# Kernel tuning notes

Measured on AMD Instinct MI355X. Metric: run time of the kernel, lower is better.

The kernel has to match this reference:

```python
import jax, jax.numpy as jnp
import numpy as np

ATTN_SCALE = 0.12
HEAD_DIM = 128


def _rms_norm(x):
    # F.rms_norm with no weight; eps defaults to machine eps of dtype
    eps = jnp.asarray(jnp.finfo(x.dtype).eps, x.dtype)
    return x * jax.lax.rsqrt(jnp.mean(x * x, axis=-1, keepdims=True) + eps)


def _rope(x):
    # x: [B, T, H, D]; standard rotary over (first-half, second-half) pairs
    T, D = x.shape[1], x.shape[-1]
    half = D // 2
    inv_freq = 1.0 / (10000.0 ** (jnp.arange(half, dtype=jnp.float32) / half))
    ang = jnp.arange(T, dtype=jnp.float32)[:, None] * inv_freq[None, :]  # [T, half]
    cos = jnp.cos(ang)[None, :, None, :].astype(x.dtype)
    sin = jnp.sin(ang)[None, :, None, :].astype(x.dtype)
    x1, x2 = x[..., :half], x[..., half:]
    return jnp.concatenate([x1 * cos - x2 * sin, x1 * sin + x2 * cos], axis=-1)


def setup_inputs() -> dict:
    key = jax.random.key(0)
    ks = jax.random.split(key, 4)
    B, T, dim, H, hd = 4, 2048, 1024, 8, HEAD_DIM
    hdim = H * hd
    std = 0.5 * dim ** (-0.5)
    bound = (3.0 ** 0.5) * std
    return {
        "x": jax.random.normal(ks[0], (B, T, dim), jnp.float32),
        "ve": jax.random.normal(ks[1], (B, T, hdim), jnp.float32),
        "qkv_w": jax.random.uniform(ks[2], (3, hdim, dim), jnp.float32, -bound, bound),
        "lambdas": jnp.array([0.5, 0.5], jnp.float32),
        "c_proj_w": jax.random.normal(ks[3], (dim, hdim), jnp.float32) * (hdim ** -0.5),
        "c_proj_b": jnp.zeros((dim,), jnp.float32),
    }


def reference(x, ve, qkv_w, lambdas, c_proj_w, c_proj_b):
    B, T, dim = x.shape
    hdim = qkv_w.shape[1]
    hd = HEAD_DIM
    H = hdim // hd
    # fused QKV projection: [B,T,3,H,hd]
    qkv = jnp.einsum('btd,ehd->bteh', x, qkv_w.reshape(3 * hdim, dim).reshape(3 * H, hd, dim).reshape(3 * hdim // hd, hd, dim))
    qkv = jnp.einsum('btd,fd->btf', x, qkv_w.reshape(3 * hdim, dim)).reshape(B, T, 3, H, hd)
    q, k, v = qkv[:, :, 0], qkv[:, :, 1], qkv[:, :, 2]  # each [B,T,H,hd]
    q, k = _rms_norm(q), _rms_norm(k)
    q, k = _rope(q), _rope(k)
    v = lambdas[0] * v + lambdas[1] * ve.reshape(B, T, H, hd)
    # causal SDPA with custom scale
    scores = jnp.einsum('bthd,bshd->bhts', q, k) * ATTN_SCALE  # [B,H,T,T]
    causal = jnp.tril(jnp.ones((T, T), dtype=bool))
    scores = jnp.where(causal[None, None], scores, jnp.finfo(scores.dtype).min)
    p = jax.nn.softmax(scores, axis=-1)
    y = jnp.einsum('bhts,bshd->bthd', p, v).reshape(B, T, hdim)
    return y @ c_proj_w.T + c_proj_b
```

## Files before the change

### kernel.cpp

```cpp
#include <hip/hip_runtime.h>
#include <math.h>

typedef unsigned short u16;
typedef short bf16x8 __attribute__((ext_vector_type(8)));
typedef u16 u16x2 __attribute__((ext_vector_type(2)));
typedef u16 u16x4 __attribute__((ext_vector_type(4)));
typedef u16 u16x8 __attribute__((ext_vector_type(8)));
typedef float f32x2 __attribute__((ext_vector_type(2)));
typedef float f32x4 __attribute__((ext_vector_type(4)));
typedef float f32x16 __attribute__((ext_vector_type(16)));

typedef __attribute__((address_space(1))) const void gvoid_t;
typedef __attribute__((address_space(3))) void lvoid_t;

__device__ __forceinline__ u16 f2bf(float f) {
  union { float f; unsigned u; } v; v.f = f;
  unsigned r = v.u + 0x7fffu + ((v.u >> 16) & 1u);
  return (u16)(r >> 16);
}
__device__ __forceinline__ float bf2f(u16 h) {
  union { unsigned u; float f; } v; v.u = ((unsigned)h) << 16;
  return v.f;
}
__device__ __forceinline__ f32x4 mfma16(bf16x8 a, bf16x8 b, f32x4 c) {
  return __builtin_amdgcn_mfma_f32_16x16x32_bf16(a, b, c, 0, 0, 0);
}
__device__ __forceinline__ f32x16 mfma32(bf16x8 a, bf16x8 b, f32x16 c) {
  return __builtin_amdgcn_mfma_f32_32x32x16_bf16(a, b, c, 0, 0, 0);
}
__device__ __forceinline__ void gload_lds16(const void* g, void* l) {
  __builtin_amdgcn_global_load_lds((gvoid_t*)g, (lvoid_t*)l, 16, 0, 0);
}
__device__ __forceinline__ unsigned cvtpk_bf16(float lo, float hi) {
  unsigned r;
  asm("v_cvt_pk_bf16_f32 %0, %1, %2" : "=v"(r) : "v"(lo), "v"(hi));
  return r;
}
__device__ __forceinline__ void pswap32(unsigned& a, unsigned& b) {
  asm("v_permlane32_swap_b32 %0, %1" : "+v"(a), "+v"(b));
}

#if __has_builtin(__builtin_amdgcn_exp2f)
#define EXPW(x) __builtin_amdgcn_exp2f(x)
#define SCALE_W 0.17312354f
#define DEFER_THR 11.5415603f
#else
#define EXPW(x) __expf(x)
#define SCALE_W 0.12f
#define DEFER_THR 8.0f
#endif

#define BAR() __builtin_amdgcn_s_barrier()
#define WAITLGKM()                          \
  asm volatile("s_waitcnt lgkmcnt(0)");     \
  __builtin_amdgcn_sched_barrier(0)
#define WAITVMC(N)                                    \
  do {                                                \
    __builtin_amdgcn_s_waitcnt(0x0F70 | (N));         \
    __builtin_amdgcn_sched_barrier(0);                \
  } while (0)

__constant__ int C_ST[24] = {15,15,7,14,14,13,13,6,12,12,11,11,5,10,10,4,9,9,8,8,3,2,1,0};
__constant__ int C_HF[24] = {0,1,-1,0,1,0,1,-1,0,1,0,1,-1,0,1,-1,0,1,0,1,-1,-1,-1,-1};

__global__ __launch_bounds__(256) void cvt_bf16_kernel(const float* __restrict__ in,
                                                       u16* __restrict__ out, int n4) {
  int i = blockIdx.x * 256 + threadIdx.x;
  if (i >= n4) return;
  f32x4 v = *(const f32x4*)(in + (size_t)i * 4);
  u16x4 o;
  o[0] = f2bf(v[0]); o[1] = f2bf(v[1]); o[2] = f2bf(v[2]); o[3] = f2bf(v[3]);
  *(u16x4*)(out + (size_t)i * 4) = o;
}

__global__ __launch_bounds__(256) void rope_tab_kernel(float* __restrict__ ct,
                                                       float* __restrict__ st) {
  int i = blockIdx.x * 256 + threadIdx.x;
  int t = i >> 6, j = i & 63;
  float inv = powf(10000.f, -(float)j * (1.0f / 64.0f));
  float ang = (float)t * inv;
  ct[i] = cosf(ang);
  st[i] = sinf(ang);
}

__global__ __launch_bounds__(512, 1) void gemm192_kernel(
    const u16* __restrict__ A, const u16* __restrict__ B, u16* __restrict__ C,
    int M, int N, int K, int nbn) {
  constexpr int WM = 128;
  constexpr int MI = 4;
  constexpr int NI = 3;
  constexpr int AR = 4;
  constexpr int NR = 7;
  __shared__ u16 Alds[2][256 * 64];
  __shared__ u16 Blds[2][192 * 64];
  int nwg = gridDim.x;
  int cpx = nwg >> 3;
  int bid = blockIdx.x;
  int swz = (bid & 7) * cpx + (bid >> 3);
  int bm = (swz & 3) + 4 * (swz / (4 * nbn));
  int bn = (swz >> 2) % nbn;
  size_t m0 = (size_t)bm * 256, n0 = (size_t)bn * 192;
  int tid = threadIdx.x, wid = tid >> 6, lane = tid & 63;
  int wr = wid >> 2, wc = wid & 3, l15 = lane & 15, l4 = lane >> 4;
  int srow = tid >> 3, sch = tid & 7;

  const u16* Abase = A + m0 * K;
  const u16* Bbase = B + n0 * K;

  f32x4 acc[8][NI];
#pragma unroll
  for (int m = 0; m < 8; m++)
#pragma unroll
    for (int n = 0; n < NI; n++) acc[m][n] = f32x4{0.f, 0.f, 0.f, 0.f};

  auto stageR = [&](int buf, int kt, int r) {
    if (r < AR) {
      int row = 64 * r + srow;
      gload_lds16(Abase + (size_t)row * K + kt * 64 + 8 * (sch ^ (row & 7)),
                  &Alds[buf][(64 * r + 8 * wid) * 64]);
    } else {
      int row = 64 * (r - AR) + srow;
      gload_lds16(Bbase + (size_t)row * K + kt * 64 + 8 * (sch ^ (row & 7)),
                  &Blds[buf][(64 * (r - AR) + 8 * wid) * 64]);
    }
  };
  auto rdA = [&](int buf, int half, bf16x8 (&a)[MI][2]) {
#pragma unroll
    for (int mi = 0; mi < MI; ++mi)
#pragma unroll
      for (int kk = 0; kk < 2; ++kk) {
        int row = WM * wr + 64 * half + 16 * mi + l15;
        a[mi][kk] = *(const bf16x8*)((const char*)(&Alds[buf][0]) + row * 128 +
                                     ((kk * 64 + 16 * l4) ^ ((row & 7) << 4)));
      }
  };
  auto rdB = [&](int buf, bf16x8 (&bb)[NI][2]) {
#pragma unroll
    for (int ni = 0; ni < NI; ++ni)
#pragma unroll
      for (int kk = 0; kk < 2; ++kk) {
        int row = 48 * wc + 16 * ni + l15;
        bb[ni][kk] = *(const bf16x8*)((const char*)(&Blds[buf][0]) + row * 128 +
                                      ((kk * 64 + 16 * l4) ^ ((row & 7) << 4)));
      }
  };

#define HALFM(AF, BF, QM)                                                 \
  do {                                                                    \
    __builtin_amdgcn_s_setprio(1);                                        \
    _Pragma("unroll") for (int mi = 0; mi < MI; ++mi)                     \
        _Pragma("unroll") for (int ni = 0; ni < NI; ++ni)                 \
            _Pragma("unroll") for (int kk = 0; kk < 2; ++kk)              \
                acc[4 * QM + mi][ni] =                                    \
        mfma16(AF[mi][kk], BF[ni][kk], acc[4 * QM + mi][ni]);             \
    __builtin_amdgcn_s_setprio(0);                                        \
  } while (0)

#pragma unroll
  for (int r = 0; r < NR; ++r) stageR(0, 0, r);
  WAITVMC(0);
  BAR();

  int nk = K >> 6;
  bf16x8 a[MI][2], b[NI][2];
  for (int t = 0; t < nk; ++t) {
    int buf = t & 1, nxt = buf ^ 1;
    bool pf = (t + 1 < nk);
    rdA(buf, 0, a);
    rdB(buf, b);
    if (pf) { stageR(nxt, t + 1, 0); stageR(nxt, t + 1, 1); stageR(nxt, t + 1, 2); stageR(nxt, t + 1, 3); }
    BAR();
    WAITLGKM();
    HALFM(a, b, 0);
    BAR();
    rdA(buf, 1, a);
    if (pf) { stageR(nxt, t + 1, 4); stageR(nxt, t + 1, 5); stageR(nxt, t + 1, 6); }
    BAR();
    WAITLGKM();
    HALFM(a, b, 1);
    WAITVMC(0);
    BAR();
  }

#pragma unroll
  for (int mi = 0; mi < 8; ++mi) {
#pragma unroll
    for (int ni = 0; ni < NI; ++ni) {
      size_t row = m0 + WM * wr + 16 * mi + 4 * l4;
      size_t col = n0 + 48 * wc + 16 * ni + l15;
#pragma unroll
      for (int i = 0; i < 4; ++i) {
        C[(row + i) * N + col] = f2bf(acc[mi][ni][i]);
      }
    }
  }
#undef HALFM
}

template <int BM, int OUTF32>
__global__ __launch_bounds__(512, 1) void gemm4p_kernel(
    const u16* __restrict__ A, const u16* __restrict__ B, void* __restrict__ C,
    const float* __restrict__ bias, int M, int N, int K, int nbn) {
  constexpr int WM = BM / 2;
  constexpr int MI = (WM / 32 > 0) ? WM / 32 : 1;
  constexpr int NACC = 2 * MI;
  constexpr int AR = BM / 64;
  constexpr int NR = AR + 4;
  constexpr int R0 = (NR + 2) / 3;
  constexpr int R1 = R0 + (NR - R0 + 1) / 2;
  __shared__ u16 Alds[2][BM * 64];
  __shared__ u16 Blds[2][256 * 64];
  int nwg = gridDim.x;
  int cpx = nwg >> 3;
  int bid = blockIdx.x;
  int swz = (bid & 7) * cpx + (bid >> 3);
  int bm = (swz & 3) + 4 * (swz / (4 * nbn));
  int bn = (swz >> 2) % nbn;
  size_t m0 = (size_t)bm * BM, n0 = (size_t)bn * 256;
  int tid = threadIdx.x, wid = tid >> 6, lane = tid & 63;
  int wr = wid >> 2, wc = wid & 3, l15 = lane & 15, l4 = lane >> 4;
  int srow = tid >> 3, sch = tid & 7;

  const u16* Abase = A + m0 * K;
  const u16* Bbase = B + n0 * K;

  f32x4 acc[NACC][4];
#pragma unroll
  for (int m = 0; m < NACC; m++)
#pragma unroll
    for (int n = 0; n < 4; n++) acc[m][n] = f32x4{0.f, 0.f, 0.f, 0.f};

  auto stageR = [&](int buf, int kt, int r) {
    if (r < AR) {
      int row = 64 * r + srow;
      gload_lds16(Abase + (size_t)row * K + kt * 64 + 8 * (sch ^ (row & 7)),
                  &Alds[buf][(64 * r + 8 * wid) * 64]);
    } else {
      int row = 64 * (r - AR) + srow;
      gload_lds16(Bbase + (size_t)row * K + kt * 64 + 8 * (sch ^ (row & 7)),
                  &Blds[buf][(64 * (r - AR) + 8 * wid) * 64]);
    }
  };
  auto rdA = [&](int buf, int qm, bf16x8 (&a)[MI][2]) {
#pragma unroll
    for (int mi = 0; mi < MI; ++mi)
#pragma unroll
      for (int kk = 0; kk < 2; ++kk) {
        int row = WM * wr + (WM / 2) * qm + 16 * mi + l15;
        a[mi][kk] = *(const bf16x8*)((const char*)(&Alds[buf][0]) + row * 128 +
                                     ((kk * 64 + 16 * l4) ^ ((row & 7) << 4)));
      }
  };
  auto rdB = [&](int buf, int qn, bf16x8 (&bb)[2][2]) {
#pragma unroll
    for (int ni = 0; ni < 2; ++ni)
#pragma unroll
      for (int kk = 0; kk < 2; ++kk) {
        int row = 64 * wc + 32 * qn + 16 * ni + l15;
        bb[ni][kk] = *(const bf16x8*)((const char*)(&Blds[buf][0]) + row * 128 +
                                      ((kk * 64 + 16 * l4) ^ ((row & 7) << 4)));
      }
  };

#define QUADX(AF, BF, QM, QN)                                             \
  do {                                                                    \
    __builtin_amdgcn_s_setprio(1);                                        \
    _Pragma("unroll") for (int mi = 0; mi < MI; ++mi)                     \
        _Pragma("unroll") for (int ni = 0; ni < 2; ++ni)                  \
            _Pragma("unroll") for (int kk = 0; kk < 2; ++kk)              \
                acc[MI * QM + mi][2 * QN + ni] =                          \
        mfma16(AF[mi][kk], BF[ni][kk], acc[MI * QM + mi][2 * QN + ni]);   \
    __builtin_amdgcn_s_setprio(0);                                        \
  } while (0)

#pragma unroll
  for (int r = 0; r < NR; ++r) stageR(0, 0, r);
  WAITVMC(0);
  BAR();

  int nk = K >> 6;
  bf16x8 a[MI][2], b0[2][2], b1[2][2];
  for (int t = 0; t < nk; ++t) {
    int buf = t & 1, nxt = buf ^ 1;
    bool pf = (t + 1 < nk);
    rdA(buf, 0, a);
    rdB(buf, 0, b0);
    if (pf) {
#pragma unroll
      for (int r = 0; r < R0; ++r) stageR(nxt, t + 1, r);
    }
    BAR();
    WAITLGKM();
    QUADX(a, b0, 0, 0);
    BAR();
    rdB(buf, 1, b1);
    if (pf) {
#pragma unroll
      for (int r = R0; r < R1; ++r) stageR(nxt, t + 1, r);
    }
    BAR();
    WAITLGKM();
    QUADX(a, b1, 0, 1);
    BAR();
    rdA(buf, 1, a);
    if (pf) {
#pragma unroll
      for (int r = R1; r < NR; ++r) stageR(nxt, t + 1, r);
    }
    BAR();
    WAITLGKM();
    QUADX(a, b0, 1, 0);
    BAR();
    QUADX(a, b1, 1, 1);
    WAITVMC(0);
    BAR();
  }

#pragma unroll
  for (int mi = 0; mi < NACC; ++mi) {
#pragma unroll
    for (int ni = 0; ni < 4; ++ni) {
      size_t row = m0 + WM * wr + 16 * mi + 4 * l4;
      size_t col = n0 + 64 * wc + 16 * ni + l15;
#pragma unroll
      for (int i = 0; i < 4; ++i) {
        float v = acc[mi][ni][i];
        if constexpr (OUTF32) {
          ((float*)C)[(row + i) * N + col] = v + bias[col];
        } else {
          ((u16*)C)[(row + i) * N + col] = f2bf(v);
        }
      }
    }
  }
#undef QUADX
}

__global__ __launch_bounds__(256) void transform_kernel(
    const u16* __restrict__ qkv, const float* __restrict__ ve,
    const float* __restrict__ lam, const float* __restrict__ ct,
    const float* __restrict__ st, u16* __restrict__ qn, u16* __restrict__ kn,
    u16* __restrict__ vt) {
  constexpr int T = 2048;
  __shared__ u16 vtile[64][136];
  int tt = blockIdx.x, bh = blockIdx.y;
  int b = bh >> 3, h = bh & 7;
  int tid = threadIdx.x, wid = tid >> 6, lane = tid & 63;
  int lsub = lane & 15, lrow = lane >> 4;
  float l0 = lam[0], l1 = lam[1];
  int d0 = 8 * lsub;
  float sgn = (lsub < 8) ? -1.f : 1.f;
  int jj = d0 & 63;
#pragma unroll
  for (int it = 0; it < 4; ++it) {
    int tl = wid * 16 + it * 4 + lrow;
    int t = tt * 64 + tl;
    size_t base = ((size_t)(b * T + t)) * 3072 + h * 128 + d0;
    u16x8 qraw = *(const u16x8*)(qkv + base);
    u16x8 kraw = *(const u16x8*)(qkv + base + 1024);
    u16x8 vraw = *(const u16x8*)(qkv + base + 2048);
    const float* vep = ve + ((size_t)(b * T + t)) * 1024 + h * 128 + d0;
    f32x4 ve0 = *(const f32x4*)(vep);
    f32x4 ve1 = *(const f32x4*)(vep + 4);
    float q[8], k[8];
    float sq = 0.f, sk = 0.f;
#pragma unroll
    for (int i = 0; i < 8; ++i) {
      q[i] = bf2f(qraw[i]); k[i] = bf2f(kraw[i]);
      sq += q[i] * q[i]; sk += k[i] * k[i];
    }
#pragma unroll
    for (int m = 1; m < 16; m <<= 1) {
      sq += __shfl_xor(sq, m);
      sk += __shfl_xor(sk, m);
    }
    float qs = rsqrtf(sq * (1.f / 128.f) + 1.1920929e-7f);
    float ks = rsqrtf(sk * (1.f / 128.f) + 1.1920929e-7f);
#pragma unroll
    for (int i = 0; i < 8; ++i) { q[i] *= qs; k[i] *= ks; }
    f32x4 c0 = *(const f32x4*)(ct + t * 64 + jj);
    f32x4 c1 = *(const f32x4*)(ct + t * 64 + jj + 4);
    f32x4 s0 = *(const f32x4*)(st + t * 64 + jj);
    f32x4 s1 = *(const f32x4*)(st + t * 64 + jj + 4);
    u16x8 oq, ok, ov;
#pragma unroll
    for (int i = 0; i < 8; ++i) {
      float qp = __shfl_xor(q[i], 8), kp = __shfl_xor(k[i], 8);
      float cc = (i < 4) ? c0[i & 3] : c1[i & 3];
      float ss = (i < 4) ? s0[i & 3] : s1[i & 3];
      oq[i] = f2bf(q[i] * cc + sgn * qp * ss);
      ok[i] = f2bf(k[i] * cc + sgn * kp * ss);
      float vv = (i < 4) ? ve0[i & 3] : ve1[i & 3];
      ov[i] = f2bf(l0 * bf2f(vraw[i]) + l1 * vv);
    }
    size_t orow = ((size_t)bh * T + t) * 128 + d0;
    *(u16x8*)(qn + orow) = oq;
    *(u16x8*)(kn + orow) = ok;
    *(u16x8*)&vtile[tl][d0] = ov;
  }
  __syncthreads();
#pragma unroll
  for (int it = 0; it < 4; ++it) {
    int ci = it * 256 + tid;
    int d = ci >> 3, c8 = ci & 7;
    u16x8 o;
#pragma unroll
    for (int u = 0; u < 8; u++) o[u] = vtile[c8 * 8 + u][d];
    *(u16x8*)(vt + ((size_t)bh * 128 + d) * T + tt * 64 + c8 * 8) = o;
  }
}

__global__ __launch_bounds__(256, 2) void attn_kernel(
    const u16* __restrict__ Qn, const u16* __restrict__ Kn,
    const u16* __restrict__ Vt, u16* __restrict__ Y,
    u16* __restrict__ pO, float* __restrict__ pml) {
  constexpr int T = 2048;
  __shared__ u16 Klds[2][64 * 128];
  __shared__ u16 Vlds[2][128 * 64];
  int bid = blockIdx.x;
  int c = bid >> 5;
  int bh = bid & 31;
  int st = C_ST[c];
  int half = C_HF[c];
  int kt0 = (half == 1) ? st + 1 : 0;
  int kt1 = (half == 0) ? st + 1 : 2 * st + 2;
  int b = bh >> 3, h = bh & 7;
  int tid = threadIdx.x, wid = tid >> 6, lane = tid & 63;
  int l31 = lane & 31, hh = lane >> 5;
  const u16* Qb = Qn + (size_t)bh * T * 128;
  const u16* Kb = Kn + (size_t)bh * T * 128;
  const u16* Vb = Vt + (size_t)bh * 128 * T;
  int q0w = st * 128 + wid * 32;
  int qmaxw = q0w + 31;
  int qg = q0w + l31;

  bf16x8 qf[8];
  {
    const u16* qr = Qb + (size_t)(q0w + l31) * 128 + 8 * hh;
#pragma unroll
    for (int ks = 0; ks < 8; ks++) qf[ks] = *(const bf16x8*)(qr + 16 * ks);
  }
  f32x16 acc[4];
#pragma unroll
  for (int mt = 0; mt < 4; mt++)
#pragma unroll
    for (int r = 0; r < 16; r++) acc[mt][r] = 0.f;
  float m_run = -1e30f, l_run = 0.f;

  auto stage = [&](int buf, int kt) {
#pragma unroll
    for (int it = 0; it < 4; ++it) {
      int id = wid * 256 + it * 64 + lane;
      int r = id >> 4, cc = id & 15;
      gload_lds16(Kb + (size_t)(kt * 64 + r) * 128 + 8 * (cc ^ (r & 7)),
                  &Klds[buf][(size_t)(wid * 256 + it * 64) * 8]);
      int rv = id >> 3, cv = id & 7;
      gload_lds16(Vb + (size_t)rv * T + kt * 64 + 8 * (cv ^ (rv & 7)),
                  &Vlds[buf][(size_t)(wid * 256 + it * 64) * 8]);
    }
  };

  int nsteps = kt1 - kt0;
  stage(0, kt0);

  for (int j = 0; j < nsteps; ++j) {
    int kt = kt0 + j;
    int cur = j & 1;
    if (j + 1 < nsteps) {
      stage(cur ^ 1, kt + 1);
      WAITVMC(8);
    } else {
      WAITVMC(0);
    }
    BAR();
    if (kt * 64 <= qmaxw) {
      const char* kb = (const char*)&Klds[cur][0];
      const char* vb = (const char*)&Vlds[cur][0];
      int rswz = (l31 & 7) << 4;
      f32x16 st0, st1;
#pragma unroll
      for (int r = 0; r < 16; r++) { st0[r] = 0.f; st1[r] = 0.f; }
      __builtin_amdgcn_s_setprio(1);
#pragma unroll
      for (int ks = 0; ks < 8; ks++) {
        bf16x8 kf0 = *(const bf16x8*)(kb + ((l31 * 256 + 32 * ks + 16 * hh) ^ rswz));
        bf16x8 kf1 = *(const bf16x8*)(kb + (((32 + l31) * 256 + 32 * ks + 16 * hh) ^ rswz));
        st0 = mfma32(kf0, qf[ks], st0);
        st1 = mfma32(kf1, qf[ks], st1);
      }
      __builtin_amdgcn_s_setprio(0);
      bool edge = (kt == (qmaxw >> 6));
      if (edge) {
#pragma unroll
        for (int r = 0; r < 16; r++) {
          int kvb = kt * 64 + (r & 3) + 8 * (r >> 2) + 4 * hh;
          if (kvb > qg) st0[r] = -1e30f;
          if (kvb + 32 > qg) st1[r] = -1e30f;
        }
      }
      float m8[8];
#pragma unroll
      for (int r = 0; r < 8; r++)
        m8[r] = fmaxf(fmaxf(st0[r], st0[r + 8]), fmaxf(st1[r], st1[r + 8]));
#pragma unroll
      for (int r = 0; r < 4; r++) m8[r] = fmaxf(m8[r], m8[r + 4]);
      float pm = fmaxf(fmaxf(m8[0], m8[1]), fmaxf(m8[2], m8[3]));
      pm = fmaxf(pm, __shfl_xor(pm, 32));
      float pmn = pm * SCALE_W;
      bool nos = __all(pmn <= m_run + DEFER_THR);
      float mnew = nos ? m_run : fmaxf(m_run, pmn);
      if (!nos) {
        float alpha = EXPW(m_run - mnew);
        l_run *= alpha;
#pragma unroll
        for (int mt = 0; mt < 4; mt++)
#pragma unroll
          for (int r = 0; r < 16; r++) acc[mt][r] *= alpha;
        m_run = mnew;
      }
      float sa = 0.f, sb = 0.f, sc = 0.f, sd = 0.f;
#pragma unroll
      for (int r = 0; r < 4; r++) {
        st0[r]      = EXPW(fmaf(st0[r],      SCALE_W, -mnew)); sa += st0[r];
        st0[r + 4]  = EXPW(fmaf(st0[r + 4],  SCALE_W, -mnew)); sb += st0[r + 4];
        st0[r + 8]  = EXPW(fmaf(st0[r + 8],  SCALE_W, -mnew)); sc += st0[r + 8];
        st0[r + 12] = EXPW(fmaf(st0[r + 12], SCALE_W, -mnew)); sd += st0[r + 12];
        st1[r]      = EXPW(fmaf(st1[r],      SCALE_W, -mnew)); sa += st1[r];
        st1[r + 4]  = EXPW(fmaf(st1[r + 4],  SCALE_W, -mnew)); sb += st1[r + 4];
        st1[r + 8]  = EXPW(fmaf(st1[r + 8],  SCALE_W, -mnew)); sc += st1[r + 8];
        st1[r + 12] = EXPW(fmaf(st1[r + 12], SCALE_W, -mnew)); sd += st1[r + 12];
      }
      float ps = (sa + sb) + (sc + sd);
      ps += __shfl_xor(ps, 32);
      l_run += ps;
      unsigned pA0[4], pB0[4], pA1[4], pB1[4];
#pragma unroll
      for (int rr = 0; rr < 4; rr++) {
        pA0[rr] = cvtpk_bf16(st0[4 * rr], st0[4 * rr + 1]);
        pB0[rr] = cvtpk_bf16(st0[4 * rr + 2], st0[4 * rr + 3]);
        pA1[rr] = cvtpk_bf16(st1[4 * rr], st1[4 * rr + 1]);
        pB1[rr] = cvtpk_bf16(st1[4 * rr + 2], st1[4 * rr + 3]);
      }
      bf16x8 pf[4];
#pragma unroll
      for (int ks2 = 0; ks2 < 4; ks2++) {
        int k1 = ks2 & 1;
        unsigned a0, b0, a1, b1;
        if (ks2 < 2) { a0 = pA0[2 * k1]; b0 = pA0[2 * k1 + 1]; a1 = pB0[2 * k1]; b1 = pB0[2 * k1 + 1]; }
        else         { a0 = pA1[2 * k1]; b0 = pA1[2 * k1 + 1]; a1 = pB1[2 * k1]; b1 = pB1[2 * k1 + 1]; }
        pswap32(a0, b0);
        pswap32(a1, b1);
        union { unsigned w[4]; bf16x8 v; } u;
        u.w[0] = a0; u.w[1] = a1; u.w[2] = b0; u.w[3] = b1;
        pf[ks2] = u.v;
      }
      __builtin_amdgcn_s_setprio(1);
#pragma unroll
      for (int mt = 0; mt < 4; mt++) {
        int row = 32 * mt + l31;
#pragma unroll
        for (int ks2 = 0; ks2 < 4; ks2++) {
          bf16x8 vf = *(const bf16x8*)(vb + ((row * 128 + 32 * ks2 + 16 * hh) ^ rswz));
          acc[mt] = mfma32(vf, pf[ks2], acc[mt]);
        }
      }
      __builtin_amdgcn_s_setprio(0);
    }
    BAR();
  }
  if (half < 0) {
    float linv = 1.f / l_run;
    size_t yrow = (size_t)b * T + q0w + l31;
    u16* yp = Y + yrow * 1024 + h * 128;
#pragma unroll
    for (int mt = 0; mt < 4; mt++) {
#pragma unroll
      for (int rr = 0; rr < 4; rr++) {
        u16x4 o;
#pragma unroll
        for (int i = 0; i < 4; i++) o[i] = f2bf(acc[mt][4 * rr + i] * linv);
        *(u16x4*)(yp + 32 * mt + 8 * rr + 4 * hh) = o;
      }
    }
  } else {
    int pidx = (((st - 8) << 5) + bh) * 2 + half;
    int qrow = wid * 32 + l31;
    u16* po = pO + (size_t)pidx * 16384 + (size_t)qrow * 128;
#pragma unroll
    for (int mt = 0; mt < 4; mt++) {
#pragma unroll
      for (int rr = 0; rr < 4; rr++) {
        u16x4 o;
#pragma unroll
        for (int i = 0; i < 4; i++) o[i] = f2bf(acc[mt][4 * rr + i]);
        *(u16x4*)(po + 32 * mt + 8 * rr + 4 * hh) = o;
      }
    }
    if (hh == 0) {
      pml[pidx * 256 + qrow] = m_run;
      pml[pidx * 256 + 128 + qrow] = l_run;
    }
  }
}

__global__ __launch_bounds__(256) void attn_merge_kernel(
    const u16* __restrict__ pO, const float* __restrict__ pml,
    u16* __restrict__ Y) {
  int blk = blockIdx.x;
  int st = 8 + (blk >> 5), bh = blk & 31;
  int b = bh >> 3, h = bh & 7;
  int tid = threadIdx.x;
  int row = tid >> 1, dh = tid & 1;
  int base = blk * 2;
  const u16* o1 = pO + (size_t)base * 16384 + (size_t)row * 128 + dh * 64;
  const u16* o2 = o1 + 16384;
  float m1 = pml[base * 256 + row], l1 = pml[base * 256 + 128 + row];
  float m2 = pml[(base + 1) * 256 + row], l2 = pml[(base + 1) * 256 + 128 + row];
  float m = fmaxf(m1, m2);
  float w1 = EXPW(m1 - m), w2 = EXPW(m2 - m);
  float inv = 1.f / (w1 * l1 + w2 * l2);
  w1 *= inv; w2 *= inv;
  u16* yp = Y + ((size_t)b * 2048 + 128 * st + row) * 1024 + h * 128 + dh * 64;
#pragma unroll
  for (int i = 0; i < 8; ++i) {
    u16x8 a = *(const u16x8*)(o1 + 8 * i);
    u16x8 cvec = *(const u16x8*)(o2 + 8 * i);
    u16x8 o;
#pragma unroll
    for (int j = 0; j < 8; ++j) o[j] = f2bf(w1 * bf2f(a[j]) + w2 * bf2f(cvec[j]));
    *(u16x8*)(yp + 8 * i) = o;
  }
}

extern "C" void kernel_launch(void* const* d_in, const int* in_sizes, int n_in,
                              void* d_out, int out_size, void* d_ws, size_t ws_size,
                              hipStream_t stream) {
  (void)in_sizes; (void)n_in; (void)out_size; (void)ws_size;
  const float* x = (const float*)d_in[0];
  const float* ve = (const float*)d_in[1];
  const float* qkvw = (const float*)d_in[2];
  const float* lam = (const float*)d_in[3];
  const float* cpw = (const float*)d_in[4];
  const float* cpb = (const float*)d_in[5];
  float* out = (float*)d_out;
  char* ws = (char*)d_ws;

  u16* xb   = (u16*)(ws + 0);
  u16* wqkv = (u16*)(ws + 16777216);
  u16* wp   = (u16*)(ws + 23068672);
  u16* qkv  = (u16*)(ws + 25165824);
  u16* qn   = (u16*)(ws + 75497472);
  u16* kn   = (u16*)(ws + 92274688);
  u16* vt   = (u16*)(ws + 109051904);
  float* ctab = (float*)(ws + 125829120);
  float* stab = (float*)(ws + 126353408);
  u16* y = xb;
  u16* pO = qkv;
  float* pml = (float*)(ws + 25165824 + 16777216);

  rope_tab_kernel<<<512, 256, 0, stream>>>(ctab, stab);
  cvt_bf16_kernel<<<8192, 256, 0, stream>>>(x, xb, 2097152);
  cvt_bf16_kernel<<<3072, 256, 0, stream>>>(qkvw, wqkv, 786432);
  cvt_bf16_kernel<<<1024, 256, 0, stream>>>(cpw, wp, 262144);
  gemm192_kernel<<<512, 512, 0, stream>>>(xb, wqkv, qkv, 8192, 3072, 1024, 16);
  transform_kernel<<<dim3(32, 32), 256, 0, stream>>>(qkv, ve, lam, ctab, stab, qn, kn, vt);
  attn_kernel<<<768, 256, 0, stream>>>(qn, kn, vt, y, pO, pml);
  attn_merge_kernel<<<256, 256, 0, stream>>>(pO, pml, y);
  gemm4p_kernel<64, 1><<<512, 512, 0, stream>>>(y, wp, out, cpb, 8192, 1024, 1024, 4);
}
```

Baseline: 203.7 us.

## Enlarge attention query tiles to 256 rows with 512-thread blocks and simplify GEMM prefetch

The attention kernel now processes 256 query rows per block with 8 waves, up from 128 rows with 4 waves. Each staged K/V tile is therefore reused by twice as many query rows, and the causal split/merge schedule, partial-output layout and merge kernel are rewritten to match. The output-projection GEMM also issues all next-tile prefetch loads at once instead of spreading them across three phases. The larger blocks halve the grid and may hurt load balance and occupancy, and issuing the whole prefetch up front can reduce overlap with compute.

```diff
diff --git a/kernel.cpp b/kernel.cpp
--- a/kernel.cpp
+++ b/kernel.cpp
@@ -60,8 +60,8 @@
     __builtin_amdgcn_sched_barrier(0);                \
   } while (0)
 
-__constant__ int C_ST[24] = {15,15,7,14,14,13,13,6,12,12,11,11,5,10,10,4,9,9,8,8,3,2,1,0};
-__constant__ int C_HF[24] = {0,1,-1,0,1,0,1,-1,0,1,0,1,-1,0,1,-1,0,1,0,1,-1,-1,-1,-1};
+__constant__ int C_ST2[12] = {7, 7, 3, 6, 6, 5, 5, 2, 4, 4, 1, 0};
+__constant__ int C_H2[12]  = {0, 1, -1, 0, 1, 0, 1, -1, 0, 1, -1, -1};
 
 __global__ __launch_bounds__(256) void cvt_bf16_kernel(const float* __restrict__ in,
                                                        u16* __restrict__ out, int n4) {
@@ -206,8 +206,6 @@
   constexpr int NACC = 2 * MI;
   constexpr int AR = BM / 64;
   constexpr int NR = AR + 4;
-  constexpr int R0 = (NR + 2) / 3;
-  constexpr int R1 = R0 + (NR - R0 + 1) / 2;
   __shared__ u16 Alds[2][BM * 64];
   __shared__ u16 Blds[2][256 * 64];
   int nwg = gridDim.x;
@@ -287,26 +285,18 @@
     rdB(buf, 0, b0);
     if (pf) {
 #pragma unroll
-      for (int r = 0; r < R0; ++r) stageR(nxt, t + 1, r);
+      for (int r = 0; r < NR; ++r) stageR(nxt, t + 1, r);
     }
     BAR();
     WAITLGKM();
     QUADX(a, b0, 0, 0);
     BAR();
     rdB(buf, 1, b1);
-    if (pf) {
-#pragma unroll
-      for (int r = R0; r < R1; ++r) stageR(nxt, t + 1, r);
-    }
     BAR();
     WAITLGKM();
     QUADX(a, b1, 0, 1);
     BAR();
     rdA(buf, 1, a);
-    if (pf) {
-#pragma unroll
-      for (int r = R1; r < NR; ++r) stageR(nxt, t + 1, r);
-    }
     BAR();
     WAITLGKM();
     QUADX(a, b0, 1, 0);
@@ -410,7 +400,7 @@
   }
 }
 
-__global__ __launch_bounds__(256, 2) void attn_kernel(
+__global__ __launch_bounds__(512, 2) void attn_kernel(
     const u16* __restrict__ Qn, const u16* __restrict__ Kn,
     const u16* __restrict__ Vt, u16* __restrict__ Y,
     u16* __restrict__ pO, float* __restrict__ pml) {
@@ -420,17 +410,18 @@
   int bid = blockIdx.x;
   int c = bid >> 5;
   int bh = bid & 31;
-  int st = C_ST[c];
-  int half = C_HF[c];
-  int kt0 = (half == 1) ? st + 1 : 0;
-  int kt1 = (half == 0) ? st + 1 : 2 * st + 2;
+  int st = C_ST2[c];
+  int hf = C_H2[c];
+  int mid = 2 * st + 2;
+  int kt0 = (hf == 1) ? mid : 0;
+  int kt1 = (hf == 0) ? mid : 4 * st + 4;
   int b = bh >> 3, h = bh & 7;
   int tid = threadIdx.x, wid = tid >> 6, lane = tid & 63;
   int l31 = lane & 31, hh = lane >> 5;
   const u16* Qb = Qn + (size_t)bh * T * 128;
   const u16* Kb = Kn + (size_t)bh * T * 128;
   const u16* Vb = Vt + (size_t)bh * 128 * T;
-  int q0w = st * 128 + wid * 32;
+  int q0w = st * 256 + wid * 32;
   int qmaxw = q0w + 31;
   int qg = q0w + l31;
 
@@ -449,14 +440,14 @@
 
   auto stage = [&](int buf, int kt) {
 #pragma unroll
-    for (int it = 0; it < 4; ++it) {
-      int id = wid * 256 + it * 64 + lane;
+    for (int it = 0; it < 2; ++it) {
+      int id = it * 512 + tid;
       int r = id >> 4, cc = id & 15;
       gload_lds16(Kb + (size_t)(kt * 64 + r) * 128 + 8 * (cc ^ (r & 7)),
-                  &Klds[buf][(size_t)(wid * 256 + it * 64) * 8]);
+                  &Klds[buf][(size_t)(it * 512 + (tid & ~63)) * 8]);
       int rv = id >> 3, cv = id & 7;
       gload_lds16(Vb + (size_t)rv * T + kt * 64 + 8 * (cv ^ (rv & 7)),
-                  &Vlds[buf][(size_t)(wid * 256 + it * 64) * 8]);
+                  &Vlds[buf][(size_t)(it * 512 + (tid & ~63)) * 8]);
     }
   };
 
@@ -468,7 +459,7 @@
     int cur = j & 1;
     if (j + 1 < nsteps) {
       stage(cur ^ 1, kt + 1);
-      WAITVMC(8);
+      WAITVMC(4);
     } else {
       WAITVMC(0);
     }
@@ -568,7 +559,7 @@
     }
     BAR();
   }
-  if (half < 0) {
+  if (hf < 0) {
     float linv = 1.f / l_run;
     size_t yrow = (size_t)b * T + q0w + l31;
     u16* yp = Y + yrow * 1024 + h * 128;
@@ -583,9 +574,10 @@
       }
     }
   } else {
-    int pidx = (((st - 8) << 5) + bh) * 2 + half;
+    int sidx = st - 4;
+    int pidx = (sidx * 32 + bh) * 2 + hf;
     int qrow = wid * 32 + l31;
-    u16* po = pO + (size_t)pidx * 16384 + (size_t)qrow * 128;
+    u16* po = pO + (size_t)pidx * 32768 + (size_t)qrow * 128;
 #pragma unroll
     for (int mt = 0; mt < 4; mt++) {
 #pragma unroll
@@ -597,8 +589,8 @@
       }
     }
     if (hh == 0) {
-      pml[pidx * 256 + qrow] = m_run;
-      pml[pidx * 256 + 128 + qrow] = l_run;
+      pml[pidx * 512 + qrow] = m_run;
+      pml[pidx * 512 + 256 + qrow] = l_run;
     }
   }
 }
@@ -607,20 +599,21 @@
     const u16* __restrict__ pO, const float* __restrict__ pml,
     u16* __restrict__ Y) {
   int blk = blockIdx.x;
-  int st = 8 + (blk >> 5), bh = blk & 31;
+  int task = blk >> 1, rh = blk & 1;
+  int st = 4 + (task >> 5), bh = task & 31;
   int b = bh >> 3, h = bh & 7;
   int tid = threadIdx.x;
-  int row = tid >> 1, dh = tid & 1;
-  int base = blk * 2;
-  const u16* o1 = pO + (size_t)base * 16384 + (size_t)row * 128 + dh * 64;
-  const u16* o2 = o1 + 16384;
-  float m1 = pml[base * 256 + row], l1 = pml[base * 256 + 128 + row];
-  float m2 = pml[(base + 1) * 256 + row], l2 = pml[(base + 1) * 256 + 128 + row];
+  int row = rh * 128 + (tid >> 1), dh = tid & 1;
+  int base = task * 2;
+  const u16* o1 = pO + (size_t)base * 32768 + (size_t)row * 128 + dh * 64;
+  const u16* o2 = o1 + 32768;
+  float m1 = pml[base * 512 + row], l1 = pml[base * 512 + 256 + row];
+  float m2 = pml[(base + 1) * 512 + row], l2 = pml[(base + 1) * 512 + 256 + row];
   float m = fmaxf(m1, m2);
   float w1 = EXPW(m1 - m), w2 = EXPW(m2 - m);
   float inv = 1.f / (w1 * l1 + w2 * l2);
   w1 *= inv; w2 *= inv;
-  u16* yp = Y + ((size_t)b * 2048 + 128 * st + row) * 1024 + h * 128 + dh * 64;
+  u16* yp = Y + ((size_t)b * 2048 + 256 * st + row) * 1024 + h * 128 + dh * 64;
 #pragma unroll
   for (int i = 0; i < 8; ++i) {
     u16x8 a = *(const u16x8*)(o1 + 8 * i);
@@ -664,7 +657,7 @@
   cvt_bf16_kernel<<<1024, 256, 0, stream>>>(cpw, wp, 262144);
   gemm192_kernel<<<512, 512, 0, stream>>>(xb, wqkv, qkv, 8192, 3072, 1024, 16);
   transform_kernel<<<dim3(32, 32), 256, 0, stream>>>(qkv, ve, lam, ctab, stab, qn, kn, vt);
-  attn_kernel<<<768, 256, 0, stream>>>(qn, kn, vt, y, pO, pml);
+  attn_kernel<<<384, 512, 0, stream>>>(qn, kn, vt, y, pO, pml);
   attn_merge_kernel<<<256, 256, 0, stream>>>(pO, pml, y);
   gemm4p_kernel<64, 1><<<512, 512, 0, stream>>>(y, wp, out, cpb, 8192, 1024, 1024, 4);
 }
```

Measured after the change: 205.8 us. Within noise of the previous version (+1.0%).
